# Kernel optimization log

Measured on AMD Instinct MI355X. Metric: run time of the kernel, lower is better.

## Reference

```python
import jax, jax.numpy as jnp
import numpy as np

B, S, H, D = 4, 8192, 8, 64  # batch, seq, heads, head_dim
M = 64                        # num random features
EPS = 1e-6


def setup_inputs() -> dict:
    key = jax.random.key(0)
    k1, k2, k3, k4 = jax.random.split(key, 4)
    qs = jax.random.normal(k1, (B, S, H, D), dtype=jnp.float32)
    ks = jax.random.normal(k2, (B, S, H, D), dtype=jnp.float32)
    vs = jax.random.normal(k3, (B, S, H, D), dtype=jnp.float32)
    proj = jax.random.normal(k4, (M, D), dtype=jnp.float32)
    return {"qs": qs, "ks": ks, "vs": vs, "proj": proj}


def _phi(x, proj):
    # stable positive softmax kernel: exp(x @ proj^T - ||x||^2/2) / sqrt(m)
    m = proj.shape[0]
    x_proj = jnp.einsum('...d,md->...m', x, proj)
    h = jnp.sum(jnp.square(x), axis=-1, keepdims=True) * 0.5
    return jnp.exp(x_proj - h) / jnp.sqrt(jnp.asarray(m, x.dtype))


def reference(qs, ks, vs, proj):
    Bq, Q, Hh, Dqk = qs.shape
    K = ks.shape[1]
    Dv = vs.shape[-1]
    # (B, S, H, D) -> (B*H, S, D)
    q = qs.transpose(0, 2, 1, 3).reshape(-1, Q, Dqk)
    k = ks.transpose(0, 2, 1, 3).reshape(-1, K, Dqk)
    v = vs.transpose(0, 2, 1, 3).reshape(-1, K, Dv)
    normalizer = 1.0 / jnp.power(jnp.asarray(Dqk, q.dtype), 0.25)
    q_prime = _phi(q * normalizer, proj)  # (B*H, Q, M)
    k_prime = _phi(k * normalizer, proj)  # (B*H, K, M)
    # fast_attend: linear-time attention
    c = jnp.concatenate([v, jnp.ones((*v.shape[:-1], 1), v.dtype)], axis=-1)  # (B*H, K, Dv+1)
    buf1 = jnp.einsum('bkm,bkc->bmc', k_prime, c)   # (B*H, M, Dv+1)
    buf2 = jnp.einsum('bqm,bmc->bqc', q_prime, buf1)  # (B*H, Q, Dv+1)
    num, den = buf2[..., :-1], buf2[..., -1]
    den = jnp.where(den < EPS, EPS, den)
    ctx = num / den[..., None]
    return ctx.reshape(Bq, Hh, Q, Dv).transpose(0, 2, 1, 3)
```

## Files before the change

### kernel.cpp

```cpp
#include <hip/hip_runtime.h>
#include <hip/hip_bf16.h>

#define S_ 8192
#define H_ 8
#define D_ 64
#define M_ 64
#define BH_ 32
#define CPK_ 80
#define MC_ (M_ * CPK_)
#define NCHQ 16
#define TILE 64
#define QTILES (S_ / NCHQ / TILE)

typedef short bf16x8 __attribute__((ext_vector_type(8)));
typedef float f32x4 __attribute__((ext_vector_type(4)));

constexpr float XS_ = 0.35355339059327373f * 1.4426950408889634f;
constexpr float HS_ = 0.34657359027997264f;
constexpr float EPS_ = 1e-6f;

__device__ __forceinline__ unsigned short f2bf(float f) {
    unsigned int u = __float_as_uint(f);
    u += 0x7FFFu + ((u >> 16) & 1u);
    return (unsigned short)(u >> 16);
}
__device__ __forceinline__ unsigned int pkbf(float lo, float hi) {
    __hip_bfloat162 t = __float22bfloat162_rn(float2{lo, hi});
    return *reinterpret_cast<unsigned int*>(&t);
}
__device__ __forceinline__ float fexp2(float x) { return __builtin_amdgcn_exp2f(x); }

#define MFMA(a, b, c) __builtin_amdgcn_mfma_f32_16x16x32_bf16((a), (b), (c), 0, 0, 0)
#define SWZ(byteoff, row) ((byteoff) ^ (((row) & 7) << 4))

#define GLDS(src, dst) __builtin_amdgcn_global_load_lds( \
    (const __attribute__((address_space(1))) void*)(src), \
    (__attribute__((address_space(3))) void*)(dst), 16, 0, 0)

__global__ void __launch_bounds__(64, 2)
fa_k(const float* __restrict__ ks, const float* __restrict__ vs,
     const float* __restrict__ proj, float* __restrict__ partial,
     int nch, int segs)
{
    __shared__ __align__(16) char bufA[8192];
    __shared__ __align__(16) char bufB[8192];

    const int chunk = blockIdx.x;
    const int bh    = blockIdx.y;
    const int b = bh >> 3, h = bh & 7;
    const int lane = threadIdx.x & 63;
    const int l15 = lane & 15, g = lane >> 4;

    const size_t rs = (size_t)H_ * D_;
    const float* kb = ks + ((size_t)b * S_ * H_ + h) * D_;
    const float* vb = vs + ((size_t)b * S_ * H_ + h) * D_;

    bf16x8 pf[4][2];
#pragma unroll
    for (int mt = 0; mt < 4; ++mt)
#pragma unroll
        for (int kk = 0; kk < 2; ++kk) {
            const float* p = proj + (mt * 16 + l15) * D_ + kk * 32 + g * 8;
            float4 a = *(const float4*)p, c = *(const float4*)(p + 4);
            union { bf16x8 v; unsigned int u[4]; } F;
            F.u[0] = pkbf(a.x, a.y); F.u[1] = pkbf(a.z, a.w);
            F.u[2] = pkbf(c.x, c.y); F.u[3] = pkbf(c.z, c.w);
            pf[mt][kk] = F.v;
        }

    bf16x8 onef = {0, 0, 0, 0, 0, 0, 0, 0};
    if (l15 == 0) {
#pragma unroll
        for (int j = 0; j < 8; ++j) onef[j] = (short)0x3F80;
    }

    f32x4 acc[4][5];
#pragma unroll
    for (int mt = 0; mt < 4; ++mt)
#pragma unroll
        for (int ci = 0; ci < 5; ++ci) acc[mt][ci] = (f32x4){0.f, 0.f, 0.f, 0.f};

    f32x4 paE[4], paO[4];
    float hrE[4], hrO[4];
    unsigned int vbu[4][4];

#define STAGE(T, BUF) do {                                                  \
    const float* krow_ = kb + (size_t)(rbase + (T) * 16 + l15) * rs;        \
    const float* vrow_ = vb + (size_t)(rbase + (T) * 16 + l15) * rs;        \
    _Pragma("unroll")                                                       \
    for (int i_ = 0; i_ < 4; ++i_) {                                        \
        int c0_ = (i_ >> 1) * 32 + (i_ & 1) * 4 + 8 * g;                    \
        GLDS(krow_ + c0_, (BUF) + i_ * 1024);                               \
        GLDS(vrow_ + c0_, (BUF) + 4096 + i_ * 1024);                        \
    } } while (0)

#define CONSUME(BUF, PA, HR) do {                                           \
    f32x4 r0_ = *(const f32x4*)((BUF) + lane * 16);                         \
    f32x4 r1_ = *(const f32x4*)((BUF) + 1024 + lane * 16);                  \
    f32x4 r2_ = *(const f32x4*)((BUF) + 2048 + lane * 16);                  \
    f32x4 r3_ = *(const f32x4*)((BUF) + 3072 + lane * 16);                  \
    float kx_[16];                                                          \
    _Pragma("unroll")                                                       \
    for (int j_ = 0; j_ < 4; ++j_) {                                        \
        kx_[j_]      = r0_[j_] * XS_;  kx_[4 + j_]  = r1_[j_] * XS_;        \
        kx_[8 + j_]  = r2_[j_] * XS_;  kx_[12 + j_] = r3_[j_] * XS_;        \
    }                                                                       \
    float sq_ = 0.f;                                                        \
    _Pragma("unroll")                                                       \
    for (int j_ = 0; j_ < 16; ++j_) sq_ += kx_[j_] * kx_[j_];               \
    sq_ += __shfl_xor(sq_, 16);                                             \
    sq_ += __shfl_xor(sq_, 32);                                             \
    float hrow_ = sq_ * HS_ + 3.0f;                                         \
    union { bf16x8 v; unsigned int u[4]; } A0_, A1_;                        \
    _Pragma("unroll")                                                       \
    for (int i_ = 0; i_ < 4; ++i_) {                                        \
        A0_.u[i_] = pkbf(kx_[2 * i_], kx_[2 * i_ + 1]);                     \
        A1_.u[i_] = pkbf(kx_[8 + 2 * i_], kx_[9 + 2 * i_]);                 \
    }                                                                       \
    _Pragma("unroll")                                                       \
    for (int mt_ = 0; mt_ < 4; ++mt_) {                                     \
        PA[mt_] = (f32x4){0.f, 0.f, 0.f, 0.f};                              \
        PA[mt_] = MFMA(A0_.v, pf[mt_][0], PA[mt_]);                         \
        PA[mt_] = MFMA(A1_.v, pf[mt_][1], PA[mt_]);                         \
    }                                                                       \
    _Pragma("unroll")                                                       \
    for (int r_ = 0; r_ < 4; ++r_) HR[r_] = __shfl(hrow_, 4 * g + r_);      \
    } while (0)

#define VHALF(BUF, I0, I1) do {                                             \
    const char* vd_ = (BUF) + 4096;                                         \
    _Pragma("unroll")                                                       \
    for (int ct_ = 0; ct_ < 4; ++ct_) {                                     \
        int c_ = ct_ * 16 + l15;                                            \
        int ic_ = ((c_ >> 5) << 1) | ((c_ >> 2) & 1);                       \
        int boff_ = ic_ * 1024 + ((c_ & 31) >> 3) * 256 + (c_ & 3) * 4      \
                  + 64 * g;                                                 \
        float e0_ = *(const float*)(vd_ + boff_);                           \
        float e1_ = *(const float*)(vd_ + boff_ + 16);                      \
        float e2_ = *(const float*)(vd_ + boff_ + 32);                      \
        float e3_ = *(const float*)(vd_ + boff_ + 48);                      \
        vbu[ct_][I0] = pkbf(e0_, e1_);                                      \
        vbu[ct_][I1] = pkbf(e2_, e3_);                                      \
    } } while (0)

#define EVREG() do {                                                        \
    _Pragma("unroll")                                                       \
    for (int mt_ = 0; mt_ < 4; ++mt_) {                                     \
        union { bf16x8 v; unsigned int u[4]; } E_;                          \
        E_.u[0] = pkbf(fexp2(paE[mt_][0] - hrE[0]),                         \
                       fexp2(paE[mt_][1] - hrE[1]));                        \
        E_.u[1] = pkbf(fexp2(paE[mt_][2] - hrE[2]),                         \
                       fexp2(paE[mt_][3] - hrE[3]));                        \
        E_.u[2] = pkbf(fexp2(paO[mt_][0] - hrO[0]),                         \
                       fexp2(paO[mt_][1] - hrO[1]));                        \
        E_.u[3] = pkbf(fexp2(paO[mt_][2] - hrO[2]),                         \
                       fexp2(paO[mt_][3] - hrO[3]));                        \
        _Pragma("unroll")                                                   \
        for (int ct_ = 0; ct_ < 4; ++ct_) {                                 \
            union { bf16x8 v; unsigned int u[4]; } B_;                      \
            B_.u[0] = vbu[ct_][0]; B_.u[1] = vbu[ct_][1];                   \
            B_.u[2] = vbu[ct_][2]; B_.u[3] = vbu[ct_][3];                   \
            acc[mt_][ct_] = MFMA(E_.v, B_.v, acc[mt_][ct_]);                \
        }                                                                   \
        acc[mt_][4] = MFMA(E_.v, onef, acc[mt_][4]);                        \
    } } while (0)

#define WAIT8 do { asm volatile("s_waitcnt vmcnt(8)" ::: "memory");         \
                   __builtin_amdgcn_sched_barrier(0); } while (0)
#define WAIT0 do { asm volatile("s_waitcnt vmcnt(0)" ::: "memory");         \
                   __builtin_amdgcn_sched_barrier(0); } while (0)

    for (int seg = 0; seg < segs; ++seg) {
        const int rbase = (chunk * segs + seg) * 128;

        STAGE(0, bufA); STAGE(1, bufB);

        WAIT8; CONSUME(bufA, paE, hrE); VHALF(bufA, 0, 1); STAGE(2, bufA);
        WAIT8; CONSUME(bufB, paO, hrO); VHALF(bufB, 2, 3); STAGE(3, bufB);
        EVREG();

        WAIT8; CONSUME(bufA, paE, hrE); VHALF(bufA, 0, 1); STAGE(4, bufA);
        WAIT8; CONSUME(bufB, paO, hrO); VHALF(bufB, 2, 3); STAGE(5, bufB);
        EVREG();

        WAIT8; CONSUME(bufA, paE, hrE); VHALF(bufA, 0, 1); STAGE(6, bufA);
        WAIT8; CONSUME(bufB, paO, hrO); VHALF(bufB, 2, 3); STAGE(7, bufB);
        EVREG();

        WAIT8; CONSUME(bufA, paE, hrE); VHALF(bufA, 0, 1);
        WAIT0; CONSUME(bufB, paO, hrO); VHALF(bufB, 2, 3);
        EVREG();
    }

    float* dst = partial + ((size_t)bh * nch + chunk) * MC_;
#pragma unroll
    for (int mt = 0; mt < 4; ++mt)
#pragma unroll
        for (int ct = 0; ct < 5; ++ct)
#pragma unroll
            for (int r = 0; r < 4; ++r)
                dst[(mt * 16 + 4 * g + r) * CPK_ + ct * 16 + l15] =
                    acc[mt][ct][r];
}

__global__ void __launch_bounds__(256)
fa_r(const float* __restrict__ partial, float* __restrict__ buf1, int nch)
{
    int e = blockIdx.x * 256 + threadIdx.x;
    if (e >= BH_ * MC_) return;
    int bh = e / MC_;
    int r  = e - bh * MC_;
    const float* src = partial + (size_t)bh * nch * MC_ + r;
    float s0 = 0.f, s1 = 0.f, s2 = 0.f, s3 = 0.f;
    int ch = 0;
    for (; ch + 4 <= nch; ch += 4) {
        s0 += src[(size_t)(ch + 0) * MC_];
        s1 += src[(size_t)(ch + 1) * MC_];
        s2 += src[(size_t)(ch + 2) * MC_];
        s3 += src[(size_t)(ch + 3) * MC_];
    }
    for (; ch < nch; ++ch) s0 += src[(size_t)ch * MC_];
    buf1[e] = (s0 + s1) + (s2 + s3);
}

__global__ void __launch_bounds__(256)
fa_q(const float* __restrict__ qs, const float* __restrict__ proj,
     const float* __restrict__ buf1, float* __restrict__ out)
{
    const int chunk = blockIdx.x;
    const int bh    = blockIdx.y;
    const int b = bh >> 3, h = bh & 7;
    const int tid = threadIdx.x, wid = tid >> 6, lane = tid & 63;
    const int l15 = lane & 15, g = lane >> 4;

    __shared__ __align__(16) char eLb[2][TILE * M_ * 2];
    __shared__ __align__(16) char b1tb[CPK_ * M_ * 2];

    const int rows = S_ / NCHQ;
    const int s0 = chunk * rows;
    const size_t rs = (size_t)H_ * D_;
    const float* qb = qs + ((size_t)b * S_ * H_ + h) * D_;

    const float* b1 = buf1 + (size_t)bh * MC_;
    for (int i = tid; i < MC_; i += 256) {
        int m = i / CPK_, c = i - m * CPK_;
        *(unsigned short*)(b1tb + SWZ(c * 128 + 2 * m, c)) = f2bf(b1[i]);
    }

    bf16x8 pf[4][2];
#pragma unroll
    for (int mt = 0; mt < 4; ++mt)
#pragma unroll
        for (int kk = 0; kk < 2; ++kk) {
            const float* p = proj + (mt * 16 + l15) * D_ + kk * 32 + g * 8;
            float4 a = *(const float4*)p, c = *(const float4*)(p + 4);
            union { bf16x8 v; unsigned int u[4]; } F;
            F.u[0] = pkbf(a.x, a.y); F.u[1] = pkbf(a.z, a.w);
            F.u[2] = pkbf(c.x, c.y); F.u[3] = pkbf(c.z, c.w);
            pf[mt][kk] = F.v;
        }
    __syncthreads();

    bf16x8 af3[5][2];
#pragma unroll
    for (int ci = 0; ci < 5; ++ci)
#pragma unroll
        for (int kk = 0; kk < 2; ++kk) {
            int c = ci * 16 + l15;
            af3[ci][kk] = *(const bf16x8*)(b1tb + SWZ(c * 128 + 16 * g + 64 * kk, c));
        }

    auto loadQ = [&](int t, float4* qp) {
        int sb = s0 + t * TILE;
        const float* qrow = qb + (size_t)(sb + wid * 16 + l15) * rs;
        qp[0] = *(const float4*)(qrow + g * 8);
        qp[1] = *(const float4*)(qrow + g * 8 + 4);
        qp[2] = *(const float4*)(qrow + 32 + g * 8);
        qp[3] = *(const float4*)(qrow + 32 + g * 8 + 4);
    };

    auto body = [&](int t, int p, const float4* qc, float4* qn) {
        if (t + 1 < QTILES) loadQ(t + 1, qn);

        float kx[16];
#pragma unroll
        for (int i = 0; i < 4; ++i) {
            kx[4 * i + 0] = qc[i].x * XS_; kx[4 * i + 1] = qc[i].y * XS_;
            kx[4 * i + 2] = qc[i].z * XS_; kx[4 * i + 3] = qc[i].w * XS_;
        }
        float sq = 0.f;
#pragma unroll
        for (int j = 0; j < 16; ++j) sq += kx[j] * kx[j];
        sq += __shfl_xor(sq, 16);
        sq += __shfl_xor(sq, 32);
        float hrow = sq * HS_ + 3.0f;

        union { bf16x8 v; unsigned int u[4]; } A0, A1;
#pragma unroll
        for (int i = 0; i < 4; ++i) {
            A0.u[i] = pkbf(kx[2 * i], kx[2 * i + 1]);
            A1.u[i] = pkbf(kx[8 + 2 * i], kx[9 + 2 * i]);
        }

        f32x4 pa[4];
#pragma unroll
        for (int mt = 0; mt < 4; ++mt) {
            pa[mt] = (f32x4){0.f, 0.f, 0.f, 0.f};
            pa[mt] = MFMA(A0.v, pf[mt][0], pa[mt]);
            pa[mt] = MFMA(A1.v, pf[mt][1], pa[mt]);
        }

        float hr[4];
#pragma unroll
        for (int r = 0; r < 4; ++r) hr[r] = __shfl(hrow, 4 * g + r);

        char* elp = eLb[p];
#pragma unroll
        for (int mt = 0; mt < 4; ++mt) {
            int m = mt * 16 + l15;
            float e0 = fexp2(pa[mt][0] - hr[0]);
            float e1 = fexp2(pa[mt][1] - hr[1]);
            float e2 = fexp2(pa[mt][2] - hr[2]);
            float e3 = fexp2(pa[mt][3] - hr[3]);
            unsigned int p01 = pkbf(e0, e1), p23 = pkbf(e2, e3);
            int q0 = wid * 16 + 4 * g;
            *(unsigned short*)(elp + SWZ((q0 + 0) * 128 + 2 * m, q0 + 0)) =
                (unsigned short)p01;
            *(unsigned short*)(elp + SWZ((q0 + 1) * 128 + 2 * m, q0 + 1)) =
                (unsigned short)(p01 >> 16);
            *(unsigned short*)(elp + SWZ((q0 + 2) * 128 + 2 * m, q0 + 2)) =
                (unsigned short)p23;
            *(unsigned short*)(elp + SWZ((q0 + 3) * 128 + 2 * m, q0 + 3)) =
                (unsigned short)(p23 >> 16);
        }
        __syncthreads();

        bf16x8 b3[2];
        {
            int qrow = wid * 16 + l15;
            b3[0] = *(const bf16x8*)(elp + SWZ(qrow * 128 + 16 * g, qrow));
            b3[1] = *(const bf16x8*)(elp + SWZ(qrow * 128 + 16 * g + 64, qrow));
        }
        f32x4 dt[5];
#pragma unroll
        for (int ci = 0; ci < 5; ++ci) {
            dt[ci] = (f32x4){0.f, 0.f, 0.f, 0.f};
            dt[ci] = MFMA(af3[ci][0], b3[0], dt[ci]);
            dt[ci] = MFMA(af3[ci][1], b3[1], dt[ci]);
        }

        float den = __shfl(dt[4][0], l15);
        float rd = 1.0f / fmaxf(den, EPS_);

        int sg = s0 + t * TILE + wid * 16 + l15;
        size_t base = (((size_t)b * S_ + sg) * H_ + h) * D_;
#pragma unroll
        for (int ci = 0; ci < 4; ++ci) {
            f32x4 o;
#pragma unroll
            for (int r = 0; r < 4; ++r) o[r] = dt[ci][r] * rd;
            *(f32x4*)(out + base + ci * 16 + 4 * g) = o;
        }
    };

    float4 qa[4], qb2[4];
    loadQ(0, qa);
    for (int t = 0; t < QTILES; t += 2) {
        body(t, 0, qa, qb2);
        body(t + 1, 1, qb2, qa);
    }
}

extern "C" void kernel_launch(void* const* d_in, const int* in_sizes, int n_in,
                              void* d_out, int out_size, void* d_ws, size_t ws_size,
                              hipStream_t stream)
{
    const float* qs   = (const float*)d_in[0];
    const float* ks   = (const float*)d_in[1];
    const float* vs   = (const float*)d_in[2];
    const float* proj = (const float*)d_in[3];
    float* out = (float*)d_out;

    int nch = 64, segs = 1;
    if ((size_t)BH_ * (size_t)(nch + 1) * MC_ * sizeof(float) > ws_size) {
        nch = 32; segs = 2;
    }

    float* partial = (float*)d_ws;
    float* buf1 = partial + (size_t)BH_ * nch * MC_;

    fa_k<<<dim3(nch, BH_), 64, 0, stream>>>(ks, vs, proj, partial, nch, segs);
    int nred = (BH_ * MC_ + 255) / 256;
    fa_r<<<dim3(nred), 256, 0, stream>>>(partial, buf1, nch);
    fa_q<<<dim3(NCHQ, BH_), 256, 0, stream>>>(qs, proj, buf1, out);
}
```

Before: 90.40 us.

## Restructure K/V pass to direct global loads with LDS-staged exp features

The K/V reduction kernel drops the async global-to-LDS double-buffer pipeline and loads K and V rows straight into registers as float4s. Exponentiated features are now written to per-wave LDS as bf16, and V is scattered transposed with a swizzle so the second MFMA reads both operands as contiguous bf16x8 vectors. Blocks grow from one wave to four, each wave owning one chunk, with the grid shrunk to match. This trades the explicit vmcnt-based overlap for more waves per block and simpler operand fetch, and adds many scalar 16-bit LDS stores for the V transpose.

```diff
diff --git a/kernel.cpp b/kernel.cpp
--- a/kernel.cpp
+++ b/kernel.cpp
@@ -33,27 +33,26 @@
 #define MFMA(a, b, c) __builtin_amdgcn_mfma_f32_16x16x32_bf16((a), (b), (c), 0, 0, 0)
 #define SWZ(byteoff, row) ((byteoff) ^ (((row) & 7) << 4))
 
-#define GLDS(src, dst) __builtin_amdgcn_global_load_lds( \
-    (const __attribute__((address_space(1))) void*)(src), \
-    (__attribute__((address_space(3))) void*)(dst), 16, 0, 0)
-
-__global__ void __launch_bounds__(64, 2)
+__global__ void __launch_bounds__(256, 2)
 fa_k(const float* __restrict__ ks, const float* __restrict__ vs,
      const float* __restrict__ proj, float* __restrict__ partial,
      int nch, int segs)
 {
-    __shared__ __align__(16) char bufA[8192];
-    __shared__ __align__(16) char bufB[8192];
-
-    const int chunk = blockIdx.x;
-    const int bh    = blockIdx.y;
+    __shared__ __align__(16) char eL[4 * 8192];
+    __shared__ __align__(16) char vL[4 * 8192];
+
+    const int bh = blockIdx.y;
     const int b = bh >> 3, h = bh & 7;
-    const int lane = threadIdx.x & 63;
+    const int tid = threadIdx.x, wid = tid >> 6, lane = tid & 63;
     const int l15 = lane & 15, g = lane >> 4;
+    const int cw = blockIdx.x * 4 + wid;
 
     const size_t rs = (size_t)H_ * D_;
     const float* kb = ks + ((size_t)b * S_ * H_ + h) * D_;
     const float* vb = vs + ((size_t)b * S_ * H_ + h) * D_;
+
+    char* eW = eL + wid * 8192;
+    char* vW = vL + wid * 8192;
 
     bf16x8 pf[4][2];
 #pragma unroll
@@ -80,119 +79,130 @@
 #pragma unroll
         for (int ci = 0; ci < 5; ++ci) acc[mt][ci] = (f32x4){0.f, 0.f, 0.f, 0.f};
 
-    f32x4 paE[4], paO[4];
-    float hrE[4], hrO[4];
-    unsigned int vbu[4][4];
-
-#define STAGE(T, BUF) do {                                                  \
-    const float* krow_ = kb + (size_t)(rbase + (T) * 16 + l15) * rs;        \
-    const float* vrow_ = vb + (size_t)(rbase + (T) * 16 + l15) * rs;        \
-    _Pragma("unroll")                                                       \
-    for (int i_ = 0; i_ < 4; ++i_) {                                        \
-        int c0_ = (i_ >> 1) * 32 + (i_ & 1) * 4 + 8 * g;                    \
-        GLDS(krow_ + c0_, (BUF) + i_ * 1024);                               \
-        GLDS(vrow_ + c0_, (BUF) + 4096 + i_ * 1024);                        \
+#define XLOAD(BASE, T, X0, X1, X2, X3) do {                                  \
+    const float* r_ = (BASE) + (size_t)(rbase + (T) * 16 + l15) * rs;        \
+    X0 = *(const float4*)(r_ + g * 8);                                       \
+    X1 = *(const float4*)(r_ + g * 8 + 4);                                   \
+    X2 = *(const float4*)(r_ + 32 + g * 8);                                  \
+    X3 = *(const float4*)(r_ + 32 + g * 8 + 4);                              \
+    } while (0)
+
+#define CONSK(T, X0, X1, X2, X3) do {                                        \
+    float kx_[16];                                                           \
+    kx_[0]=X0.x*XS_; kx_[1]=X0.y*XS_; kx_[2]=X0.z*XS_; kx_[3]=X0.w*XS_;      \
+    kx_[4]=X1.x*XS_; kx_[5]=X1.y*XS_; kx_[6]=X1.z*XS_; kx_[7]=X1.w*XS_;      \
+    kx_[8]=X2.x*XS_; kx_[9]=X2.y*XS_; kx_[10]=X2.z*XS_; kx_[11]=X2.w*XS_;    \
+    kx_[12]=X3.x*XS_; kx_[13]=X3.y*XS_; kx_[14]=X3.z*XS_; kx_[15]=X3.w*XS_;  \
+    float sq_ = 0.f;                                                         \
+    _Pragma("unroll")                                                        \
+    for (int j_ = 0; j_ < 16; ++j_) sq_ += kx_[j_] * kx_[j_];                \
+    sq_ += __shfl_xor(sq_, 16);                                              \
+    sq_ += __shfl_xor(sq_, 32);                                              \
+    float hrow_ = sq_ * HS_ + 3.0f;                                          \
+    union { bf16x8 v; unsigned int u[4]; } A0_, A1_;                         \
+    _Pragma("unroll")                                                        \
+    for (int i_ = 0; i_ < 4; ++i_) {                                         \
+        A0_.u[i_] = pkbf(kx_[2 * i_], kx_[2 * i_ + 1]);                      \
+        A1_.u[i_] = pkbf(kx_[8 + 2 * i_], kx_[9 + 2 * i_]);                  \
+    }                                                                        \
+    f32x4 pa_[4];                                                            \
+    _Pragma("unroll")                                                        \
+    for (int mt_ = 0; mt_ < 4; ++mt_) {                                      \
+        pa_[mt_] = (f32x4){0.f, 0.f, 0.f, 0.f};                              \
+        pa_[mt_] = MFMA(A0_.v, pf[mt_][0], pa_[mt_]);                        \
+        pa_[mt_] = MFMA(A1_.v, pf[mt_][1], pa_[mt_]);                        \
+    }                                                                        \
+    float hr_[4];                                                            \
+    _Pragma("unroll")                                                        \
+    for (int r_ = 0; r_ < 4; ++r_) hr_[r_] = __shfl(hrow_, 4 * g + r_);      \
+    _Pragma("unroll")                                                        \
+    for (int mt_ = 0; mt_ < 4; ++mt_) {                                      \
+        unsigned int u0_ = pkbf(fexp2(pa_[mt_][0] - hr_[0]),                 \
+                                fexp2(pa_[mt_][1] - hr_[1]));                \
+        unsigned int u1_ = pkbf(fexp2(pa_[mt_][2] - hr_[2]),                 \
+                                fexp2(pa_[mt_][3] - hr_[3]));                \
+        *(unsigned long long*)(eW + ((T) >> 1) * 4096 + mt_ * 1024           \
+                               + lane * 16 + ((T) & 1) * 8) =                \
+            (unsigned long long)u0_ | ((unsigned long long)u1_ << 32);       \
     } } while (0)
 
-#define CONSUME(BUF, PA, HR) do {                                           \
-    f32x4 r0_ = *(const f32x4*)((BUF) + lane * 16);                         \
-    f32x4 r1_ = *(const f32x4*)((BUF) + 1024 + lane * 16);                  \
-    f32x4 r2_ = *(const f32x4*)((BUF) + 2048 + lane * 16);                  \
-    f32x4 r3_ = *(const f32x4*)((BUF) + 3072 + lane * 16);                  \
-    float kx_[16];                                                          \
-    _Pragma("unroll")                                                       \
-    for (int j_ = 0; j_ < 4; ++j_) {                                        \
-        kx_[j_]      = r0_[j_] * XS_;  kx_[4 + j_]  = r1_[j_] * XS_;        \
-        kx_[8 + j_]  = r2_[j_] * XS_;  kx_[12 + j_] = r3_[j_] * XS_;        \
-    }                                                                       \
-    float sq_ = 0.f;                                                        \
-    _Pragma("unroll")                                                       \
-    for (int j_ = 0; j_ < 16; ++j_) sq_ += kx_[j_] * kx_[j_];               \
-    sq_ += __shfl_xor(sq_, 16);                                             \
-    sq_ += __shfl_xor(sq_, 32);                                             \
-    float hrow_ = sq_ * HS_ + 3.0f;                                         \
-    union { bf16x8 v; unsigned int u[4]; } A0_, A1_;                        \
-    _Pragma("unroll")                                                       \
-    for (int i_ = 0; i_ < 4; ++i_) {                                        \
-        A0_.u[i_] = pkbf(kx_[2 * i_], kx_[2 * i_ + 1]);                     \
-        A1_.u[i_] = pkbf(kx_[8 + 2 * i_], kx_[9 + 2 * i_]);                 \
-    }                                                                       \
-    _Pragma("unroll")                                                       \
-    for (int mt_ = 0; mt_ < 4; ++mt_) {                                     \
-        PA[mt_] = (f32x4){0.f, 0.f, 0.f, 0.f};                              \
-        PA[mt_] = MFMA(A0_.v, pf[mt_][0], PA[mt_]);                         \
-        PA[mt_] = MFMA(A1_.v, pf[mt_][1], PA[mt_]);                         \
-    }                                                                       \
-    _Pragma("unroll")                                                       \
-    for (int r_ = 0; r_ < 4; ++r_) HR[r_] = __shfl(hrow_, 4 * g + r_);      \
-    } while (0)
-
-#define VHALF(BUF, I0, I1) do {                                             \
-    const char* vd_ = (BUF) + 4096;                                         \
-    _Pragma("unroll")                                                       \
-    for (int ct_ = 0; ct_ < 4; ++ct_) {                                     \
-        int c_ = ct_ * 16 + l15;                                            \
-        int ic_ = ((c_ >> 5) << 1) | ((c_ >> 2) & 1);                       \
-        int boff_ = ic_ * 1024 + ((c_ & 31) >> 3) * 256 + (c_ & 3) * 4      \
-                  + 64 * g;                                                 \
-        float e0_ = *(const float*)(vd_ + boff_);                           \
-        float e1_ = *(const float*)(vd_ + boff_ + 16);                      \
-        float e2_ = *(const float*)(vd_ + boff_ + 32);                      \
-        float e3_ = *(const float*)(vd_ + boff_ + 48);                      \
-        vbu[ct_][I0] = pkbf(e0_, e1_);                                      \
-        vbu[ct_][I1] = pkbf(e2_, e3_);                                      \
+#define VSCAT(T, X0, X1, X2, X3) do {                                        \
+    char* vp_ = vW + ((T) >> 1) * 4096;                                      \
+    int slot2_ = 2 * (((l15 >> 2) & 3) * 8 + 4 * ((T) & 1) + (l15 & 3));     \
+    float vv_[16];                                                           \
+    vv_[0]=X0.x; vv_[1]=X0.y; vv_[2]=X0.z; vv_[3]=X0.w;                      \
+    vv_[4]=X1.x; vv_[5]=X1.y; vv_[6]=X1.z; vv_[7]=X1.w;                      \
+    vv_[8]=X2.x; vv_[9]=X2.y; vv_[10]=X2.z; vv_[11]=X2.w;                    \
+    vv_[12]=X3.x; vv_[13]=X3.y; vv_[14]=X3.z; vv_[15]=X3.w;                  \
+    _Pragma("unroll")                                                        \
+    for (int p2_ = 0; p2_ < 4; ++p2_) {                                      \
+        int cA_ = g * 8 + 2 * p2_;                                           \
+        unsigned int pA_ = pkbf(vv_[2 * p2_], vv_[2 * p2_ + 1]);             \
+        *(unsigned short*)(vp_ + cA_ * 64 + (slot2_ ^ ((cA_ & 3) << 4))) =   \
+            (unsigned short)pA_;                                             \
+        int cB_ = cA_ + 1;                                                   \
+        *(unsigned short*)(vp_ + cB_ * 64 + (slot2_ ^ ((cB_ & 3) << 4))) =   \
+            (unsigned short)(pA_ >> 16);                                     \
+        int cC_ = 32 + cA_;                                                  \
+        unsigned int pB_ = pkbf(vv_[8 + 2 * p2_], vv_[9 + 2 * p2_]);         \
+        *(unsigned short*)(vp_ + cC_ * 64 + (slot2_ ^ ((cC_ & 3) << 4))) =   \
+            (unsigned short)pB_;                                             \
+        int cD_ = cC_ + 1;                                                   \
+        *(unsigned short*)(vp_ + cD_ * 64 + (slot2_ ^ ((cD_ & 3) << 4))) =   \
+            (unsigned short)(pB_ >> 16);                                     \
     } } while (0)
 
-#define EVREG() do {                                                        \
-    _Pragma("unroll")                                                       \
-    for (int mt_ = 0; mt_ < 4; ++mt_) {                                     \
-        union { bf16x8 v; unsigned int u[4]; } E_;                          \
-        E_.u[0] = pkbf(fexp2(paE[mt_][0] - hrE[0]),                         \
-                       fexp2(paE[mt_][1] - hrE[1]));                        \
-        E_.u[1] = pkbf(fexp2(paE[mt_][2] - hrE[2]),                         \
-                       fexp2(paE[mt_][3] - hrE[3]));                        \
-        E_.u[2] = pkbf(fexp2(paO[mt_][0] - hrO[0]),                         \
-                       fexp2(paO[mt_][1] - hrO[1]));                        \
-        E_.u[3] = pkbf(fexp2(paO[mt_][2] - hrO[2]),                         \
-                       fexp2(paO[mt_][3] - hrO[3]));                        \
-        _Pragma("unroll")                                                   \
-        for (int ct_ = 0; ct_ < 4; ++ct_) {                                 \
-            union { bf16x8 v; unsigned int u[4]; } B_;                      \
-            B_.u[0] = vbu[ct_][0]; B_.u[1] = vbu[ct_][1];                   \
-            B_.u[2] = vbu[ct_][2]; B_.u[3] = vbu[ct_][3];                   \
-            acc[mt_][ct_] = MFMA(E_.v, B_.v, acc[mt_][ct_]);                \
-        }                                                                   \
-        acc[mt_][4] = MFMA(E_.v, onef, acc[mt_][4]);                        \
+#define EVP(P) do {                                                          \
+    bf16x8 eA_[4], vB_[4];                                                   \
+    _Pragma("unroll")                                                        \
+    for (int mt_ = 0; mt_ < 4; ++mt_)                                        \
+        eA_[mt_] = *(const bf16x8*)(eW + (P) * 4096 + mt_ * 1024             \
+                                    + lane * 16);                            \
+    _Pragma("unroll")                                                        \
+    for (int ct_ = 0; ct_ < 4; ++ct_) {                                      \
+        int c_ = ct_ * 16 + l15;                                             \
+        vB_[ct_] = *(const bf16x8*)(vW + (P) * 4096 + c_ * 64                \
+                                    + ((16 * g) ^ ((c_ & 3) << 4)));         \
+    }                                                                        \
+    _Pragma("unroll")                                                        \
+    for (int mt_ = 0; mt_ < 4; ++mt_) {                                      \
+        _Pragma("unroll")                                                    \
+        for (int ct_ = 0; ct_ < 4; ++ct_)                                    \
+            acc[mt_][ct_] = MFMA(eA_[mt_], vB_[ct_], acc[mt_][ct_]);         \
+        acc[mt_][4] = MFMA(eA_[mt_], onef, acc[mt_][4]);                     \
     } } while (0)
 
-#define WAIT8 do { asm volatile("s_waitcnt vmcnt(8)" ::: "memory");         \
-                   __builtin_amdgcn_sched_barrier(0); } while (0)
-#define WAIT0 do { asm volatile("s_waitcnt vmcnt(0)" ::: "memory");         \
-                   __builtin_amdgcn_sched_barrier(0); } while (0)
-
     for (int seg = 0; seg < segs; ++seg) {
-        const int rbase = (chunk * segs + seg) * 128;
-
-        STAGE(0, bufA); STAGE(1, bufB);
-
-        WAIT8; CONSUME(bufA, paE, hrE); VHALF(bufA, 0, 1); STAGE(2, bufA);
-        WAIT8; CONSUME(bufB, paO, hrO); VHALF(bufB, 2, 3); STAGE(3, bufB);
-        EVREG();
-
-        WAIT8; CONSUME(bufA, paE, hrE); VHALF(bufA, 0, 1); STAGE(4, bufA);
-        WAIT8; CONSUME(bufB, paO, hrO); VHALF(bufB, 2, 3); STAGE(5, bufB);
-        EVREG();
-
-        WAIT8; CONSUME(bufA, paE, hrE); VHALF(bufA, 0, 1); STAGE(6, bufA);
-        WAIT8; CONSUME(bufB, paO, hrO); VHALF(bufB, 2, 3); STAGE(7, bufB);
-        EVREG();
-
-        WAIT8; CONSUME(bufA, paE, hrE); VHALF(bufA, 0, 1);
-        WAIT0; CONSUME(bufB, paO, hrO); VHALF(bufB, 2, 3);
-        EVREG();
-    }
-
-    float* dst = partial + ((size_t)bh * nch + chunk) * MC_;
+#pragma unroll
+        for (int g2 = 0; g2 < 2; ++g2) {
+            const int rbase = cw * (128 * segs) + seg * 128 + g2 * 64;
+            float4 a0, a1, a2, a3, b0, b1, b2, b3;
+
+            XLOAD(kb, 0, a0, a1, a2, a3);
+            XLOAD(kb, 1, b0, b1, b2, b3);
+            CONSK(0, a0, a1, a2, a3);
+            XLOAD(kb, 2, a0, a1, a2, a3);
+            CONSK(1, b0, b1, b2, b3);
+            XLOAD(kb, 3, b0, b1, b2, b3);
+            CONSK(2, a0, a1, a2, a3);
+            CONSK(3, b0, b1, b2, b3);
+            __builtin_amdgcn_sched_barrier(0);
+
+            XLOAD(vb, 0, a0, a1, a2, a3);
+            XLOAD(vb, 1, b0, b1, b2, b3);
+            VSCAT(0, a0, a1, a2, a3);
+            XLOAD(vb, 2, a0, a1, a2, a3);
+            VSCAT(1, b0, b1, b2, b3);
+            XLOAD(vb, 3, b0, b1, b2, b3);
+            EVP(0);
+            VSCAT(2, a0, a1, a2, a3);
+            VSCAT(3, b0, b1, b2, b3);
+            EVP(1);
+            __builtin_amdgcn_sched_barrier(0);
+        }
+    }
+
+    float* dst = partial + ((size_t)bh * nch + cw) * MC_;
 #pragma unroll
     for (int mt = 0; mt < 4; ++mt)
 #pragma unroll
@@ -381,15 +391,16 @@
     const float* proj = (const float*)d_in[3];
     float* out = (float*)d_out;
 
-    int nch = 64, segs = 1;
+    int segs = 1, nch = 64;
     if ((size_t)BH_ * (size_t)(nch + 1) * MC_ * sizeof(float) > ws_size) {
-        nch = 32; segs = 2;
-    }
+        segs = 2; nch = 32;
+    }
+    int gx = 16 / segs;
 
     float* partial = (float*)d_ws;
     float* buf1 = partial + (size_t)BH_ * nch * MC_;
 
-    fa_k<<<dim3(nch, BH_), 64, 0, stream>>>(ks, vs, proj, partial, nch, segs);
+    fa_k<<<dim3(gx, BH_), 256, 0, stream>>>(ks, vs, proj, partial, nch, segs);
     int nred = (BH_ * MC_ + 255) / 256;
     fa_r<<<dim3(nred), 256, 0, stream>>>(partial, buf1, nch);
     fa_q<<<dim3(NCHQ, BH_), 256, 0, stream>>>(qs, proj, buf1, out);
```

After: 83.75 us. 7.4% less time.
